# Kernel optimization log

Hardware: AMD Instinct MI355X
Metric: run time of the kernel (lower is better)

The kernel has to match this reference:

```python
import jax, jax.numpy as jnp
import numpy as np
from jax import lax

B, S = 128, 8192
MIN_PATCH, MAX_PATCH = 2, 16
LOOKAHEAD = 8
THRESHOLD = 2.9
PAD_TOKEN = 0
VOCAB = 256
MAXP = -(-S // MIN_PATCH)  # static upper bound on #patches (torch trims to batch max; we pad+mask)


def setup_inputs() -> dict:
    key = jax.random.key(0)
    tokens = jax.random.randint(key, (B, S), 0, VOCAB, dtype=jnp.int32)
    return {"tokens": tokens}


def _entropy_all_starts(seq):
    # ent[j] = Shannon entropy (bits) of window seq[j : min(S, j + LOOKAHEAD)]
    # Using c_i = multiplicity of element i within its window:
    #   H = -(1/L) * sum_i log2(c_i / L)   (each unique value contributes c_i identical terms)
    pos = jnp.arange(S)[:, None] + jnp.arange(LOOKAHEAD)[None, :]          # [S, L]
    valid = pos < S
    w = seq[jnp.minimum(pos, S - 1)]                                       # [S, L]
    eq = (w[:, :, None] == w[:, None, :]) & valid[:, :, None] & valid[:, None, :]
    counts = eq.sum(-1).astype(jnp.float32)                                # [S, L] c_i (0 where invalid)
    L = valid.sum(-1).astype(jnp.float32)                                  # [S]
    logs = jnp.where(valid, jnp.log2(jnp.maximum(counts, 1.0) / jnp.maximum(L, 1.0)[:, None]), 0.0)
    return -logs.sum(-1) / jnp.maximum(L, 1.0)                             # [S]


def _patch_one(seq):
    ent = _entropy_all_starts(seq)
    stop = ent >= THRESHOLD
    # next_stop[j] = smallest j' >= j with stop[j'], else S (padded so next_stop[S] = S)
    vals = jnp.concatenate([jnp.where(stop, jnp.arange(S, dtype=jnp.int32), S),
                            jnp.array([S], dtype=jnp.int32)])
    next_stop = lax.associative_scan(jnp.minimum, vals, reverse=True)      # [S+1]
    i_all = jnp.arange(S, dtype=jnp.int32)
    # inner while-loop closed form: grow from min_patch until stop/seq-end/max_patch
    sizes = jnp.minimum(MAX_PATCH, next_stop[jnp.minimum(i_all + MIN_PATCH, S)] - i_all)  # [S]

    def step(i, _):
        ok = i < S
        sz = jnp.where(ok, sizes[jnp.minimum(i, S - 1)], 1)
        return i + sz, (i, sz, ok)

    _, (starts, szs, mask) = lax.scan(step, jnp.int32(0), None, length=MAXP)
    return starts, szs, mask


def reference(tokens):
    starts, szs, mask = jax.vmap(_patch_one)(tokens)                       # [B, MAXP]
    lane = jnp.arange(MAX_PATCH, dtype=jnp.int32)
    idx = starts[:, :, None] + lane[None, None, :]                         # [B, MAXP, MAX_PATCH]
    within = (lane[None, None, :] < szs[:, :, None]) & mask[:, :, None]
    g = jnp.take_along_axis(tokens, jnp.minimum(idx, S - 1).reshape(tokens.shape[0], -1), axis=1)
    patches = jnp.where(within, g.reshape(tokens.shape[0], MAXP, MAX_PATCH), PAD_TOKEN)
    return patches, mask
```

## Files before the change

### kernel.cpp

```cpp
#include <hip/hip_runtime.h>
#include <stdint.h>

#define SEQ  8192
#define NB   128
#define MAXP 4096
#define NT   512
#define RED  2
#define NCH  256

__device__ __forceinline__ bool haszero8(uint64_t v) {
    return ((v - 0x0101010101010101ULL) & ~v & 0x8080808080808080ULL) != 0ULL;
}
__device__ __forceinline__ bool distinct8(uint64_t w) {
    uint64_t r1 = (w >> 8)  | (w << 56);
    uint64_t r2 = (w >> 16) | (w << 48);
    uint64_t r3 = (w >> 24) | (w << 40);
    uint64_t r4 = (w >> 32) | (w << 32);
    return !(haszero8(w ^ r1) | haszero8(w ^ r2) | haszero8(w ^ r3) | haszero8(w ^ r4));
}
__device__ __forceinline__ uint32_t pack4(int4 v) {
    return (uint32_t)(v.x & 255) | ((uint32_t)(v.y & 255) << 8) |
           ((uint32_t)(v.z & 255) << 16) | ((uint32_t)(v.w & 255) << 24);
}
__device__ __forceinline__ uint32_t bsel16(uint4 f, uint32_t b) {
    uint32_t w01 = (b & 4u) ? f.y : f.x;
    uint32_t w23 = (b & 4u) ? f.w : f.z;
    uint32_t w   = (b & 8u) ? w23 : w01;
    return (w >> ((b & 3u) << 3)) & 255u;
}
__device__ __forceinline__ uint32_t packexit(uint32_t pa, uint32_t pb) {
#if __has_builtin(__builtin_amdgcn_perm)
    return __builtin_amdgcn_perm(pb, pa, 0x06040200u);
#else
    return (pa & 0xFFu) | (((pa >> 16) & 0xFFu) << 8) |
           ((pb & 0xFFu) << 16) | (((pb >> 16) & 0xFFu) << 24);
#endif
}
__device__ __forceinline__ uint4 comp16(uint4 g, uint4 f) {
    uint4 r;
#if __has_builtin(__builtin_amdgcn_perm)
    #define C16W(fw, out) do { \
        uint32_t sel = (fw) & 0x07070707u; \
        uint32_t lo = __builtin_amdgcn_perm(g.y, g.x, sel); \
        uint32_t hi = __builtin_amdgcn_perm(g.w, g.z, sel); \
        uint32_t m = ((fw) & 0x08080808u) >> 3; m = (m << 8) - m; \
        out = (lo & ~m) | (hi & m); } while (0)
    C16W(f.x, r.x); C16W(f.y, r.y); C16W(f.z, r.z); C16W(f.w, r.w);
    #undef C16W
#else
    #define C16B(fw, out) do { uint32_t o = 0; \
        o |= bsel16(g, (fw) & 15u); \
        o |= bsel16(g, ((fw) >> 8) & 15u) << 8; \
        o |= bsel16(g, ((fw) >> 16) & 15u) << 16; \
        o |= bsel16(g, ((fw) >> 24) & 15u) << 24; \
        out = o; } while (0)
    C16B(f.x, r.x); C16B(f.y, r.y); C16B(f.z, r.z); C16B(f.w, r.w);
    #undef C16B
#endif
    return r;
}
__device__ __forceinline__ int psize(const uint32_t* stopb, int p) {
    int bp = p + 2, w = bp >> 5;
    uint64_t comb = (uint64_t)stopb[w] | ((uint64_t)stopb[w + 1] << 32);
    uint32_t win14 = (uint32_t)(comb >> (bp & 31)) & 0x3FFFu;
    return win14 ? (2 + __builtin_ctz(win14)) : min(16, SEQ - p);
}

__global__ __launch_bounds__(NT) void ep_fused(const int* __restrict__ tokens,
                                               int* __restrict__ out) {
    __shared__ uint32_t tok32[2056];
    __shared__ uint32_t stopb[258];
    __shared__ uint32_t st16[NCH * 9];
    __shared__ uint32_t exitf32[NCH * 4];
    __shared__ uint8_t  entry_s[NCH];
    __shared__ uint16_t pbase_s[NCH];
    __shared__ uint16_t starts_s[4100];
    __shared__ int S_s[2];

    const int bx = blockIdx.x;
    const int b = bx >> 1, qc = bx & 1;
    const int tid = threadIdx.x;

    {
        const int4* t4 = (const int4*)(tokens + (size_t)b * SEQ);
        #pragma unroll
        for (int k = 0; k < 4; ++k) { int g = k * NT + tid; tok32[g] = pack4(t4[g]); }
        if (tid < 8) tok32[2048 + tid] = 0u;
        if (tid < 2) stopb[256 + tid] = 0u;
    }
    __syncthreads();

    {
        const int base = tid * 4;
        uint64_t win = (uint64_t)tok32[base] | ((uint64_t)tok32[base + 1] << 32);
        uint32_t bits = 0;
        #pragma unroll
        for (int k = 0; k < 4; ++k) {
            uint32_t nx = tok32[base + 2 + k];
            #pragma unroll
            for (int m = 0; m < 4; ++m) {
                if (distinct8(win)) bits |= (1u << (k * 4 + m));
                win = (win >> 8) | ((uint64_t)(nx & 255u) << 56);
                nx >>= 8;
            }
        }
        if (tid == NT - 1) bits &= 0x1FFu;
        uint32_t other = (uint32_t)__shfl_xor((int)bits, 1);
        if ((tid & 1) == 0) stopb[tid >> 1] = (bits & 0xFFFFu) | (other << 16);
    }
    __syncthreads();

    if (tid < NCH) {
        const int c = tid;
        const uint64_t W = (uint64_t)stopb[c] | ((uint64_t)stopb[c + 1] << 32);
        const int gb = c * 32;
        uint32_t p0 = 0, p1 = 0, p2 = 0, p3 = 0, p4 = 0, p5 = 0, p6 = 0, p7 = 0;
        #pragma unroll
        for (int rel = 31; rel >= 0; --rel) {
            uint32_t win14 = (uint32_t)(W >> (rel + 2)) & 0x3FFFu;
            int sz = win14 ? (2 + __builtin_ctz(win14)) : min(16, SEQ - (gb + rel));
            int nxt = rel + sz;
            uint32_t stv;
            if (nxt >= 32) {
                stv = (uint32_t)(nxt - 32) | 0x100u;
            } else {
                int s = sz - 1;
                uint32_t q01 = (s & 2) ? p1 : p0;
                uint32_t q23 = (s & 2) ? p3 : p2;
                uint32_t q45 = (s & 2) ? p5 : p4;
                uint32_t q67 = (s & 2) ? p7 : p6;
                uint32_t qa  = (s & 4) ? q23 : q01;
                uint32_t qb  = (s & 4) ? q67 : q45;
                uint32_t q   = (s & 8) ? qb : qa;
                uint32_t sel = (s & 1) ? (q >> 16) : (q & 0xFFFFu);
                stv = sel + 0x100u;
            }
            p7 = (p7 << 16) | (p6 >> 16);
            p6 = (p6 << 16) | (p5 >> 16);
            p5 = (p5 << 16) | (p4 >> 16);
            p4 = (p4 << 16) | (p3 >> 16);
            p3 = (p3 << 16) | (p2 >> 16);
            p2 = (p2 << 16) | (p1 >> 16);
            p1 = (p1 << 16) | (p0 >> 16);
            p0 = (p0 << 16) | stv;
        }
        uint32_t* st = st16 + c * 9;
        st[0] = p0; st[1] = p1; st[2] = p2; st[3] = p3;
        st[4] = p4; st[5] = p5; st[6] = p6; st[7] = p7;
        exitf32[c * 4 + 0] = packexit(p0, p1);
        exitf32[c * 4 + 1] = packexit(p2, p3);
        exitf32[c * 4 + 2] = packexit(p4, p5);
        exitf32[c * 4 + 3] = packexit(p6, p7);
    }
    __syncthreads();

    if (tid < 64) {
        const uint4* xf4 = (const uint4*)exitf32;
        uint4 f0 = xf4[tid * 4], f1 = xf4[tid * 4 + 1],
              f2 = xf4[tid * 4 + 2], f3 = xf4[tid * 4 + 3];
        uint4 g = comp16(f1, f0);
        g = comp16(f2, g);
        g = comp16(f3, g);
        #pragma unroll
        for (int d = 1; d < 64; d <<= 1) {
            uint4 o;
            o.x = (uint32_t)__shfl_up((int)g.x, d);
            o.y = (uint32_t)__shfl_up((int)g.y, d);
            o.z = (uint32_t)__shfl_up((int)g.z, d);
            o.w = (uint32_t)__shfl_up((int)g.w, d);
            if (tid >= d) g = comp16(g, o);
        }
        uint4 E;
        E.x = (uint32_t)__shfl_up((int)g.x, 1);
        E.y = (uint32_t)__shfl_up((int)g.y, 1);
        E.z = (uint32_t)__shfl_up((int)g.z, 1);
        E.w = (uint32_t)__shfl_up((int)g.w, 1);
        if (tid == 0) E = make_uint4(0x03020100u, 0x07060504u, 0x0B0A0908u, 0x0F0E0D0Cu);
        uint32_t e0 = E.x & 255u;
        uint32_t e1 = bsel16(f0, e0);
        uint32_t e2 = bsel16(f1, e1);
        uint32_t e3 = bsel16(f2, e2);
        entry_s[tid * 4 + 0] = (uint8_t)e0;
        entry_s[tid * 4 + 1] = (uint8_t)e1;
        entry_s[tid * 4 + 2] = (uint8_t)e2;
        entry_s[tid * 4 + 3] = (uint8_t)e3;
        uint32_t w0 = st16[(tid * 4 + 0) * 9 + (e0 >> 1)];
        uint32_t w1 = st16[(tid * 4 + 1) * 9 + (e1 >> 1)];
        uint32_t w2 = st16[(tid * 4 + 2) * 9 + (e2 >> 1)];
        uint32_t w3 = st16[(tid * 4 + 3) * 9 + (e3 >> 1)];
        int c0 = (int)(((w0 >> ((e0 & 1) * 16)) & 0xFFFFu) >> 8);
        int c1 = (int)(((w1 >> ((e1 & 1) * 16)) & 0xFFFFu) >> 8);
        int c2 = (int)(((w2 >> ((e2 & 1) * 16)) & 0xFFFFu) >> 8);
        int c3 = (int)(((w3 >> ((e3 & 1) * 16)) & 0xFFFFu) >> 8);
        int s = c0 + c1 + c2 + c3;
        int incl = s;
        #pragma unroll
        for (int d = 1; d < 64; d <<= 1) { int o = __shfl_up(incl, d); if (tid >= d) incl += o; }
        int excl = incl - s;
        pbase_s[tid * 4 + 0] = (uint16_t)excl;
        pbase_s[tid * 4 + 1] = (uint16_t)(excl + c0);
        pbase_s[tid * 4 + 2] = (uint16_t)(excl + c0 + c1);
        pbase_s[tid * 4 + 3] = (uint16_t)(excl + c0 + c1 + c2);
        if (tid == 63) S_s[0] = incl;
    }
    __syncthreads();

    if (tid < NCH) {
        int pb = (int)pbase_s[tid];
        int p = tid * 32 + (int)entry_s[tid];
        const int lim = tid * 32 + 32;
        while (p < lim) {
            starts_s[pb++] = (uint16_t)p;
            p += psize(stopb, p);
        }
    }
    {
        const int P = S_s[0];
        for (int i = P + tid; i < 4098; i += NT) starts_s[i] = (uint16_t)SEQ;
    }
    __syncthreads();

    {
        int* outp = out + (size_t)b * (MAXP * 16);
        int* outm = out + (size_t)NB * MAXP * 16 + (size_t)b * MAXP;
        const int j = tid & 3;
        #pragma unroll
        for (int it = 0; it < (MAXP / RED) / (NT / 4); ++it) {
            const int p = qc * (MAXP / RED) + it * (NT / 4) + (tid >> 2);
            const int st = (int)starts_s[p];
            const int sz = (int)starts_s[p + 1] - st;
            const int base = (st >> 2) + j;
            const uint32_t sh = (uint32_t)(st & 3) * 8u;
            uint32_t lo = tok32[base], hi = tok32[base + 1];
            uint32_t pk = (uint32_t)((((uint64_t)hi << 32) | lo) >> sh);
            int rem = sz - 4 * j;
            rem = (rem < 0) ? 0 : (rem > 4 ? 4 : rem);
            pk &= (uint32_t)((1ULL << (8 * rem)) - 1ULL);
            ((int4*)outp)[(size_t)p * 4 + j] =
                make_int4((int)(pk & 255u), (int)((pk >> 8) & 255u),
                          (int)((pk >> 16) & 255u), (int)(pk >> 24));
        }
        {
            const int p4 = qc * (MAXP / RED) + tid * 4;
            const uint32_t* s32 = (const uint32_t*)starts_s;
            uint32_t a = s32[p4 >> 1], bw = s32[(p4 >> 1) + 1];
            ((int4*)(outm + qc * (MAXP / RED)))[tid] =
                make_int4((a & 0xFFFFu) < SEQ ? 1 : 0, (a >> 16) < SEQ ? 1 : 0,
                          (bw & 0xFFFFu) < SEQ ? 1 : 0, (bw >> 16) < SEQ ? 1 : 0);
        }
    }
}

extern "C" void kernel_launch(void* const* d_in, const int* in_sizes, int n_in,
                              void* d_out, int out_size, void* d_ws, size_t ws_size,
                              hipStream_t stream) {
    const int* tokens = (const int*)d_in[0];
    int* out = (int*)d_out;
    ep_fused<<<dim3(NB * RED), dim3(NT), 0, stream>>>(tokens, out);
}
```

Measured before the change: 21.03 us.

## Double threads per block and keep stop bits in registers during patch walk

Raises the block size from 512 to 1024 threads. Each thread now loads half as many tokens and computes 8 stop bits instead of 16, and two shuffles assemble the 32-bit stop words. The per-chunk patch walk preloads its 64-bit stop window into registers instead of re-reading shared memory on each step. The output loop automatically gets fewer iterations per thread, and the mask write is guarded so only the first 512 threads run it. In exchange, the larger block puts more register pressure on each thread and may lower occupancy, and the serial phases still use only 256 or 64 threads.

```diff
diff --git a/kernel.cpp b/kernel.cpp
--- a/kernel.cpp
+++ b/kernel.cpp
@@ -4,7 +4,7 @@
 #define SEQ  8192
 #define NB   128
 #define MAXP 4096
-#define NT   512
+#define NT   1024
 #define RED  2
 #define NCH  256
 
@@ -59,12 +59,6 @@
 #endif
     return r;
 }
-__device__ __forceinline__ int psize(const uint32_t* stopb, int p) {
-    int bp = p + 2, w = bp >> 5;
-    uint64_t comb = (uint64_t)stopb[w] | ((uint64_t)stopb[w + 1] << 32);
-    uint32_t win14 = (uint32_t)(comb >> (bp & 31)) & 0x3FFFu;
-    return win14 ? (2 + __builtin_ctz(win14)) : min(16, SEQ - p);
-}
 
 __global__ __launch_bounds__(NT) void ep_fused(const int* __restrict__ tokens,
                                                int* __restrict__ out) {
@@ -84,29 +78,33 @@
     {
         const int4* t4 = (const int4*)(tokens + (size_t)b * SEQ);
         #pragma unroll
-        for (int k = 0; k < 4; ++k) { int g = k * NT + tid; tok32[g] = pack4(t4[g]); }
+        for (int k = 0; k < 2; ++k) { int g = k * NT + tid; tok32[g] = pack4(t4[g]); }
         if (tid < 8) tok32[2048 + tid] = 0u;
         if (tid < 2) stopb[256 + tid] = 0u;
     }
     __syncthreads();
 
     {
-        const int base = tid * 4;
+        const int base = tid * 2;
         uint64_t win = (uint64_t)tok32[base] | ((uint64_t)tok32[base + 1] << 32);
+        uint32_t nx0 = tok32[base + 2], nx1 = tok32[base + 3];
         uint32_t bits = 0;
         #pragma unroll
-        for (int k = 0; k < 4; ++k) {
-            uint32_t nx = tok32[base + 2 + k];
-            #pragma unroll
-            for (int m = 0; m < 4; ++m) {
-                if (distinct8(win)) bits |= (1u << (k * 4 + m));
-                win = (win >> 8) | ((uint64_t)(nx & 255u) << 56);
-                nx >>= 8;
-            }
-        }
-        if (tid == NT - 1) bits &= 0x1FFu;
-        uint32_t other = (uint32_t)__shfl_xor((int)bits, 1);
-        if ((tid & 1) == 0) stopb[tid >> 1] = (bits & 0xFFFFu) | (other << 16);
+        for (int m = 0; m < 4; ++m) {
+            if (distinct8(win)) bits |= (1u << m);
+            win = (win >> 8) | ((uint64_t)(nx0 & 255u) << 56);
+            nx0 >>= 8;
+        }
+        #pragma unroll
+        for (int m = 4; m < 8; ++m) {
+            if (distinct8(win)) bits |= (1u << m);
+            win = (win >> 8) | ((uint64_t)(nx1 & 255u) << 56);
+            nx1 >>= 8;
+        }
+        if (tid == NT - 1) bits &= 0x1u;
+        uint32_t a = bits | ((uint32_t)__shfl_xor((int)bits, 1) << 8);
+        uint32_t w32 = a | ((uint32_t)__shfl_xor((int)a, 2) << 16);
+        if ((tid & 3) == 0) stopb[tid >> 2] = w32;
     }
     __syncthreads();
 
@@ -206,12 +204,15 @@
     __syncthreads();
 
     if (tid < NCH) {
-        int pb = (int)pbase_s[tid];
-        int p = tid * 32 + (int)entry_s[tid];
-        const int lim = tid * 32 + 32;
-        while (p < lim) {
-            starts_s[pb++] = (uint16_t)p;
-            p += psize(stopb, p);
+        const int c = tid;
+        const uint64_t W = (uint64_t)stopb[c] | ((uint64_t)stopb[c + 1] << 32);
+        const int gb = c * 32;
+        int pb = (int)pbase_s[c];
+        int rel = (int)entry_s[c];
+        while (rel < 32) {
+            starts_s[pb++] = (uint16_t)(gb + rel);
+            uint32_t win14 = (uint32_t)(W >> (rel + 2)) & 0x3FFFu;
+            rel += win14 ? (2 + __builtin_ctz(win14)) : min(16, SEQ - (gb + rel));
         }
     }
     {
@@ -240,7 +241,7 @@
                 make_int4((int)(pk & 255u), (int)((pk >> 8) & 255u),
                           (int)((pk >> 16) & 255u), (int)(pk >> 24));
         }
-        {
+        if (tid < (MAXP / RED) / 4) {
             const int p4 = qc * (MAXP / RED) + tid * 4;
             const uint32_t* s32 = (const uint32_t*)starts_s;
             uint32_t a = s32[p4 >> 1], bw = s32[(p4 >> 1) + 1];
```

After: 20.58 us. -2.2%, faster.
